# Kernel optimization log

Measured on AMD Instinct MI355X. Metric: run time of the kernel, lower is better.

The kernel has to match this reference:

```python
import jax, jax.numpy as jnp
import numpy as np

NUM_AA, EMB, H = 20, 16, 128
IN1 = 1 + 2 + 4 * EMB  # 67: theta, sin/cos phi, 4-residue context
IN2 = 2 + 2 + 4 * EMB  # 68: sin/cos phi_i, sin/cos phi_{i+1}, context


def setup_inputs() -> dict:
    key = jax.random.key(0)
    ks = jax.random.split(key, 12)
    B, L = 64, 4096
    R = jax.random.normal(ks[0], (B, L, 3), dtype=jnp.float32)
    seq = jax.random.randint(ks[1], (B, L), 0, NUM_AA)
    def lin(k, i, o):
        kw, kb = jax.random.split(k)
        s = 1.0 / np.sqrt(i)
        return (jax.random.uniform(kw, (i, o), jnp.float32, -s, s),
                jax.random.uniform(kb, (o,), jnp.float32, -s, s))
    emb = jax.random.normal(ks[2], (NUM_AA, EMB), dtype=jnp.float32)
    tp_W1, tp_b1 = lin(ks[3], IN1, H)
    tp_W2, tp_b2 = lin(ks[4], H, H)
    tp_W3, tp_b3 = lin(ks[5], H, 1)
    pp_W1, pp_b1 = lin(ks[6], IN2, H)
    pp_W2, pp_b2 = lin(ks[7], H, H)
    pp_W3, pp_b3 = lin(ks[8], H, 1)
    return dict(R=R, seq=seq, emb=emb,
                tp_W1=tp_W1, tp_b1=tp_b1, tp_W2=tp_W2, tp_b2=tp_b2, tp_W3=tp_W3, tp_b3=tp_b3,
                pp_W1=pp_W1, pp_b1=pp_b1, pp_W2=pp_W2, pp_b2=pp_b2, pp_W3=pp_W3, pp_b3=pp_b3)


def _mlp(x, W1, b1, W2, b2, W3, b3):
    h = jax.nn.relu(x @ W1 + b1)
    h = jax.nn.relu(h @ W2 + b2)
    return x @ 0.0 if False else h @ W3 + b3


def _bond_angles(R):
    # angle at residue i+1 of triplet (i, i+1, i+2) -> (B, L-2)
    u1 = R[:, :-2] - R[:, 1:-1]
    u2 = R[:, 2:] - R[:, 1:-1]
    c = jnp.cross(u1, u2)
    return jnp.arctan2(jnp.linalg.norm(c, axis=-1), jnp.sum(u1 * u2, axis=-1))


def _torsions(R):
    # dihedral of quadruplet (i..i+3) -> (B, L-3)
    b1 = R[:, 1:-2] - R[:, :-3]
    b2 = R[:, 2:-1] - R[:, 1:-2]
    b3 = R[:, 3:] - R[:, 2:-1]
    n1 = jnp.cross(b1, b2)
    n2 = jnp.cross(b2, b3)
    b2n = b2 / (jnp.linalg.norm(b2, axis=-1, keepdims=True) + 1e-8)
    x = jnp.sum(n1 * n2, axis=-1)
    y = jnp.sum(jnp.cross(n1, n2) * b2n, axis=-1)
    return jnp.arctan2(y, x)


def reference(R, seq, emb,
              tp_W1, tp_b1, tp_W2, tp_b2, tp_W3, tp_b3,
              pp_W1, pp_b1, pp_W2, pp_b2, pp_W3, pp_b3):
    B, L, _ = R.shape
    e = emb[seq]                                   # (B, L, EMB)
    theta = _bond_angles(R)                        # (B, L-2)
    phi = _torsions(R)                             # (B, L-3)
    sc_phi = jnp.stack([jnp.sin(phi), jnp.cos(phi)], axis=-1)  # (B, L-3, 2)
    theta_in = jnp.cos(theta[:, :L - 3])           # use_cos_theta=True
    ctx = jnp.concatenate([e[:, :-3], e[:, 1:-2], e[:, 2:-1], e[:, 3:]], axis=-1)  # (B, L-3, 4*EMB)
    x1 = jnp.concatenate([theta_in[..., None], sc_phi, ctx], axis=-1)  # (B, L-3, 67)
    E1 = _mlp(x1, tp_W1, tp_b1, tp_W2, tp_b2, tp_W3, tp_b3)[..., 0].sum(axis=1)
    x2 = jnp.concatenate([sc_phi[:, :-1], sc_phi[:, 1:], ctx[:, :-1]], axis=-1)    # (B, L-4, 68)
    E2 = _mlp(x2, pp_W1, pp_b1, pp_W2, pp_b2, pp_W3, pp_b3)[..., 0].sum(axis=1)
    return E1 + E2
```

## Files before the change

### kernel.cpp

```cpp
#include <hip/hip_runtime.h>

#define L_   4096
#define LIM0 4093
#define LIM1 4092

typedef short s16x8 __attribute__((ext_vector_type(8)));
typedef float f32x4 __attribute__((ext_vector_type(4)));

__device__ __forceinline__ unsigned short f2bf(float f) {
    union { float f; unsigned int u; } v; v.f = f;
    unsigned int r = v.u + 0x7FFFu + ((v.u >> 16) & 1u);
    return (unsigned short)(r >> 16);
}

__device__ __forceinline__ unsigned int cvt_pk_bf16(float lo, float hi) {
    unsigned int r;
    asm("v_cvt_pk_bf16_f32 %0, %1, %2" : "=v"(r) : "v"(lo), "v"(hi));
    return r;
}

struct F3 { float x, y, z; };
__device__ __forceinline__ F3 ld3(const float* p) { return F3{p[0], p[1], p[2]}; }
__device__ __forceinline__ F3 sub3(F3 a, F3 b) { return F3{a.x-b.x, a.y-b.y, a.z-b.z}; }
__device__ __forceinline__ F3 cross3(F3 a, F3 b) {
    return F3{a.y*b.z - a.z*b.y, a.z*b.x - a.x*b.z, a.x*b.y - a.y*b.x};
}
__device__ __forceinline__ float dot3(F3 a, F3 b) { return a.x*b.x + a.y*b.y + a.z*b.z; }

__device__ __forceinline__ void torsion(F3 a, F3 b, F3 c, F3 d, float& sn, float& cs) {
    F3 v1 = sub3(b, a), v2 = sub3(c, b), v3 = sub3(d, c);
    F3 n1 = cross3(v1, v2), n2 = cross3(v2, v3);
    float x = dot3(n1, n2);
    F3 m = cross3(n1, n2);
    float bn = sqrtf(dot3(v2, v2)) + 1e-8f;
    float y = dot3(m, v2) / bn;
    float inv = rsqrtf(x*x + y*y + 1e-30f);
    sn = y * inv; cs = x * inv;
}

#define MFMA16 __builtin_amdgcn_mfma_f32_16x16x32_bf16

__global__ __launch_bounds__(256) void ss_mlp(
    const float* __restrict__ R, const int* __restrict__ seq, const float* __restrict__ emb,
    const float* __restrict__ tpW1, const float* __restrict__ tpb1,
    const float* __restrict__ tpW2, const float* __restrict__ tpb2,
    const float* __restrict__ ppW1, const float* __restrict__ ppb1,
    const float* __restrict__ ppW2, const float* __restrict__ ppb2,
    float* __restrict__ wsp) {

    __shared__ __align__(16) unsigned short H1s[64*128];
    __shared__ __align__(16) uint4 embs4[40];
    __shared__ unsigned int feats[520];

    const int b = blockIdx.y, mode = blockIdx.z, bx = blockIdx.x;
    const int lim = mode ? LIM1 : LIM0;
    const float* W1  = mode ? ppW1 : tpW1;
    const float* Bi1 = mode ? ppb1 : tpb1;
    const float* W2  = mode ? ppW2 : tpW2;
    const float* Bi2 = mode ? ppb2 : tpb2;

    const int t = threadIdx.x;
    const int w = t >> 6, l = t & 63, g = l >> 4, ln = l & 15;
    const int lw = ln & 7;
    const size_t bL = (size_t)b * L_;
    const int base = bx * 256;
    const int* seqb = seq + bL;

    int aa_c[8];
    #pragma unroll
    for (int pt = 0; pt < 4; pt++)
        #pragma unroll
        for (int kk = 0; kk < 2; kk++)
            aa_c[pt*2+kk] = seqb[min(base + pt*16 + ln + kk*2 + (g>>1), L_-1)];

    {
        const int pc = min(base + t, lim - 1);
        const float* Rp = R + ((size_t)(bL + pc)) * 3;
        F3 p0 = ld3(Rp), p1 = ld3(Rp+3), p2 = ld3(Rp+6), p3 = ld3(Rp+9);
        float sp, cp; torsion(p0, p1, p2, p3, sp, cp);
        if (mode == 0) {
            F3 u1 = sub3(p0, p1), u2 = sub3(p2, p1);
            F3 cr = cross3(u1, u2);
            float d = dot3(u1, u2);
            float ct = d * rsqrtf(d*d + dot3(cr, cr) + 1e-30f);
            feats[2*t]   = cvt_pk_bf16(ct, sp);
            feats[2*t+1] = cvt_pk_bf16(cp, 1.0f);
        } else {
            feats[t] = cvt_pk_bf16(sp, cp);
            if (t == 0) {
                const int pc2 = min(base + 256, lim - 1);
                const float* R2 = R + ((size_t)(bL + pc2)) * 3;
                F3 q0 = ld3(R2), q1 = ld3(R2+3), q2 = ld3(R2+6), q3 = ld3(R2+9);
                float s2, c2; torsion(q0, q1, q2, q3, s2, c2);
                feats[256] = cvt_pk_bf16(s2, c2);
            }
        }
    }

    if (t < 40) {
        const float* ep = emb + (t >> 1) * 16 + (t & 1) * 8;
        embs4[t] = make_uint4(cvt_pk_bf16(ep[0], ep[1]), cvt_pk_bf16(ep[2], ep[3]),
                              cvt_pk_bf16(ep[4], ep[5]), cvt_pk_bf16(ep[6], ep[7]));
    }

    s16x8 a1f[2][3]; s16x8 a2f[2][4];
    float bb2[2][4];
    #pragma unroll
    for (int mt = 0; mt < 2; mt++) {
        const int hc = w*32 + mt*16 + ln;
        #pragma unroll
        for (int kk = 0; kk < 3; kk++)
            #pragma unroll
            for (int j = 0; j < 8; j++) {
                const int c = kk*32 + g*8 + j;
                int kp;
                if (mode) kp = (c < 64) ? c + 4 : ((c < 68) ? c - 64 : ((c == 68) ? -2 : -1));
                else      kp = (c < 64) ? c + 3 : ((c < 67) ? c - 64 : ((c == 67) ? -2 : -1));
                float wv = (kp == -1) ? 0.f : ((kp == -2) ? Bi1[hc] : W1[kp*128 + hc]);
                a1f[mt][kk][j] = (short)f2bf(wv);
            }
        #pragma unroll
        for (int kk = 0; kk < 4; kk++)
            #pragma unroll
            for (int j = 0; j < 8; j++)
                a2f[mt][kk][j] = (short)f2bf(W2[(kk*32 + g*8 + j)*128 + hc]);
        #pragma unroll
        for (int i = 0; i < 4; i++) bb2[mt][i] = Bi2[w*32 + mt*16 + g*4 + i];
    }

    __syncthreads();

    float s[2][4] = {{0.f,0.f,0.f,0.f},{0.f,0.f,0.f,0.f}};

    #pragma unroll
    for (int it = 0; it < 4; it++) {
        const int pos0 = base + it*64;

        int aa_n[8];
        if (it < 3) {
            #pragma unroll
            for (int pt = 0; pt < 4; pt++)
                #pragma unroll
                for (int kk = 0; kk < 2; kk++)
                    aa_n[pt*2+kk] = seqb[min(pos0 + 64 + pt*16 + ln + kk*2 + (g>>1), L_-1)];
        }

        #pragma unroll
        for (int pt = 0; pt < 4; pt++) {
            const int row = pt*16 + ln;
            const int fidx = it*64 + row;
            s16x8 b0 = *(const s16x8*)&embs4[aa_c[pt*2+0]*2 + (g&1)];
            s16x8 b1 = *(const s16x8*)&embs4[aa_c[pt*2+1]*2 + (g&1)];
            unsigned int f0, f1, f2c;
            if (mode) { f0 = feats[fidx]; f1 = feats[fidx+1]; f2c = 0x00003F80u; }
            else      { f0 = feats[2*fidx]; f1 = feats[2*fidx+1]; f2c = 0u; }
            const bool gz = (g == 0);
            union { unsigned int u[4]; s16x8 v; } fb;
            fb.u[0] = gz ? f0 : 0u; fb.u[1] = gz ? f1 : 0u;
            fb.u[2] = gz ? f2c : 0u; fb.u[3] = 0u;

            f32x4 c0 = {0.f,0.f,0.f,0.f}, c1 = {0.f,0.f,0.f,0.f};
            c0 = MFMA16(a1f[0][0], b0, c0, 0, 0, 0);
            c1 = MFMA16(a1f[1][0], b0, c1, 0, 0, 0);
            c0 = MFMA16(a1f[0][1], b1, c0, 0, 0, 0);
            c1 = MFMA16(a1f[1][1], b1, c1, 0, 0, 0);
            c0 = MFMA16(a1f[0][2], fb.v, c0, 0, 0, 0);
            c1 = MFMA16(a1f[1][2], fb.v, c1, 0, 0, 0);

            unsigned short* hb = H1s + row*128;
            uint2 u;
            u.x = cvt_pk_bf16(fmaxf(c0[0], 0.f), fmaxf(c0[1], 0.f));
            u.y = cvt_pk_bf16(fmaxf(c0[2], 0.f), fmaxf(c0[3], 0.f));
            *(uint2*)(hb + ((((w*4) + (g>>1)) ^ lw) << 3) + (g&1)*4) = u;
            u.x = cvt_pk_bf16(fmaxf(c1[0], 0.f), fmaxf(c1[1], 0.f));
            u.y = cvt_pk_bf16(fmaxf(c1[2], 0.f), fmaxf(c1[3], 0.f));
            *(uint2*)(hb + ((((w*4 + 2) + (g>>1)) ^ lw) << 3) + (g&1)*4) = u;
        }
        __syncthreads();

        #pragma unroll
        for (int pt = 0; pt < 4; pt++) {
            const int row = pt*16 + ln;
            const unsigned short* hbase = H1s + row*128;
            f32x4 d0 = {0.f,0.f,0.f,0.f}, d1 = {0.f,0.f,0.f,0.f};
            #pragma unroll
            for (int kk = 0; kk < 4; kk++) {
                s16x8 bf = *(const s16x8*)(hbase + (((kk*4 + g) ^ lw) << 3));
                d0 = MFMA16(a2f[0][kk], bf, d0, 0, 0, 0);
                d1 = MFMA16(a2f[1][kk], bf, d1, 0, 0, 0);
            }
            if (pos0 + row < lim) {
                #pragma unroll
                for (int i = 0; i < 4; i++) {
                    s[0][i] += fmaxf(d0[i] + bb2[0][i], 0.f);
                    s[1][i] += fmaxf(d1[i] + bb2[1][i], 0.f);
                }
            }
        }
        __syncthreads();

        if (it < 3) {
            #pragma unroll
            for (int j = 0; j < 8; j++) aa_c[j] = aa_n[j];
        }
    }

    #pragma unroll
    for (int mt = 0; mt < 2; mt++)
        #pragma unroll
        for (int i = 0; i < 4; i++) {
            float v = s[mt][i];
            v += __shfl_xor(v, 1, 64); v += __shfl_xor(v, 2, 64);
            v += __shfl_xor(v, 4, 64); v += __shfl_xor(v, 8, 64);
            s[mt][i] = v;
        }
    if (ln == 0) {
        float* dst = wsp + (((size_t)(b*2 + mode)*16 + bx) << 7) + w*32;
        *(f32x4*)(dst +  0 + g*4) = f32x4{s[0][0], s[0][1], s[0][2], s[0][3]};
        *(f32x4*)(dst + 16 + g*4) = f32x4{s[1][0], s[1][1], s[1][2], s[1][3]};
    }
}

__global__ void ss_finish(const float* __restrict__ wsp,
                          const float* __restrict__ tpW3, const float* __restrict__ tpb3,
                          const float* __restrict__ ppW3, const float* __restrict__ ppb3,
                          float* __restrict__ out) {
    const int b = blockIdx.x, t = threadIdx.x;
    const float* p0 = wsp + ((size_t)(b*2 + 0) * 16) * 128;
    const float* p1 = wsp + ((size_t)(b*2 + 1) * 16) * 128;
    float a0 = 0.f, a1 = 0.f;
    #pragma unroll
    for (int bx = 0; bx < 16; bx++) {
        a0 += p0[bx*128 + t];
        a1 += p1[bx*128 + t];
    }
    float v = a0 * tpW3[t] + a1 * ppW3[t];
    #pragma unroll
    for (int off = 1; off < 64; off <<= 1) v += __shfl_xor(v, off, 64);
    __shared__ float ps[2];
    if ((t & 63) == 0) ps[t >> 6] = v;
    __syncthreads();
    if (t == 0) out[b] = ps[0] + ps[1] + 4093.f * tpb3[0] + 4092.f * ppb3[0];
}

extern "C" void kernel_launch(void* const* d_in, const int* in_sizes, int n_in,
                              void* d_out, int out_size, void* d_ws, size_t ws_size,
                              hipStream_t stream) {
    (void)in_sizes; (void)n_in; (void)out_size; (void)ws_size;
    const float* R    = (const float*)d_in[0];
    const int*   seq  = (const int*)d_in[1];
    const float* emb  = (const float*)d_in[2];
    const float* tpW1 = (const float*)d_in[3];
    const float* tpb1 = (const float*)d_in[4];
    const float* tpW2 = (const float*)d_in[5];
    const float* tpb2 = (const float*)d_in[6];
    const float* tpW3 = (const float*)d_in[7];
    const float* tpb3 = (const float*)d_in[8];
    const float* ppW1 = (const float*)d_in[9];
    const float* ppb1 = (const float*)d_in[10];
    const float* ppW2 = (const float*)d_in[11];
    const float* ppb2 = (const float*)d_in[12];
    const float* ppW3 = (const float*)d_in[13];
    const float* ppb3 = (const float*)d_in[14];
    float* wsp = (float*)d_ws;

    ss_mlp<<<dim3(16, 64, 2), 256, 0, stream>>>(R, seq, emb,
                                                tpW1, tpb1, tpW2, tpb2,
                                                ppW1, ppb1, ppW2, ppb2, wsp);
    ss_finish<<<64, 128, 0, stream>>>(wsp, tpW3, tpb3, ppW3, ppb3, (float*)d_out);
}
```

Measured before the change: 52.34 us.

## Precompute geometry features and bf16 weight fragments in a separate prologue kernel

Adds a pre-pass kernel that computes bond-angle and torsion features once per position into global memory, and converts the embedding table and W1/W2 into per-lane bf16 MFMA fragments. The MLP kernel then loads ready-made fragments and features instead of recomputing torsions and converting weights in every block. It also doubles each block's span to 512 positions, halving the grid and the number of partial sums. The cost is an extra kernel launch, global round-trips for features and fragments, per-row global feature and embedding loads in place of shared-memory reads, and a larger shared H1 buffer.

```diff
diff --git a/kernel.cpp b/kernel.cpp
--- a/kernel.cpp
+++ b/kernel.cpp
@@ -6,12 +6,6 @@
 
 typedef short s16x8 __attribute__((ext_vector_type(8)));
 typedef float f32x4 __attribute__((ext_vector_type(4)));
-
-__device__ __forceinline__ unsigned short f2bf(float f) {
-    union { float f; unsigned int u; } v; v.f = f;
-    unsigned int r = v.u + 0x7FFFu + ((v.u >> 16) & 1u);
-    return (unsigned short)(r >> 16);
-}
 
 __device__ __forceinline__ unsigned int cvt_pk_bf16(float lo, float hi) {
     unsigned int r;
@@ -40,154 +34,158 @@
 
 #define MFMA16 __builtin_amdgcn_mfma_f32_16x16x32_bf16
 
+__global__ __launch_bounds__(256) void ss_pre(
+    const float* __restrict__ R, uint2* __restrict__ featG,
+    const float* __restrict__ emb, uint4* __restrict__ embbfG,
+    const float* __restrict__ tpW1, const float* __restrict__ tpb1,
+    const float* __restrict__ tpW2,
+    const float* __restrict__ ppW1, const float* __restrict__ ppb1,
+    const float* __restrict__ ppW2,
+    uint4* __restrict__ wfragG) {
+    const int t = threadIdx.x;
+    if (blockIdx.x == 16) {
+        if (blockIdx.y != 0) return;
+        if (t < 40) {
+            const float* ep = emb + (t >> 1) * 16 + (t & 1) * 8;
+            embbfG[t] = make_uint4(cvt_pk_bf16(ep[0], ep[1]), cvt_pk_bf16(ep[2], ep[3]),
+                                   cvt_pk_bf16(ep[4], ep[5]), cvt_pk_bf16(ep[6], ep[7]));
+        }
+        for (int F = t; F < 7168; F += 256) {
+            int l = F & 63, q = F >> 6;
+            int kkL = q % 7; q /= 7;
+            int mt = q & 1; q >>= 1;
+            int w = q & 3, mode = q >> 2;
+            int g = l >> 4, ln = l & 15;
+            int hc = w*32 + mt*16 + ln;
+            const float* W1  = mode ? ppW1 : tpW1;
+            const float* Bi1 = mode ? ppb1 : tpb1;
+            const float* W2  = mode ? ppW2 : tpW2;
+            float v[8];
+            #pragma unroll
+            for (int j = 0; j < 8; j++) {
+                if (kkL < 3) {
+                    int c = kkL*32 + g*8 + j;
+                    int kp;
+                    if (mode) kp = (c < 64) ? c + 4 : ((c < 68) ? c - 64 : ((c == 68) ? -2 : -1));
+                    else      kp = (c < 64) ? c + 3 : ((c == 64) ? 0 : ((c == 65) ? -2 :
+                                   ((c == 66) ? 1 : ((c == 67) ? 2 : -1))));
+                    v[j] = (kp == -1) ? 0.f : ((kp == -2) ? Bi1[hc] : W1[kp*128 + hc]);
+                } else {
+                    v[j] = W2[((kkL - 3)*32 + g*8 + j)*128 + hc];
+                }
+            }
+            wfragG[F] = make_uint4(cvt_pk_bf16(v[0], v[1]), cvt_pk_bf16(v[2], v[3]),
+                                   cvt_pk_bf16(v[4], v[5]), cvt_pk_bf16(v[6], v[7]));
+        }
+        return;
+    }
+    const int p = blockIdx.x * 256 + t;
+    const int b = blockIdx.y;
+    if (p >= LIM0) return;
+    const float* Rp = R + ((size_t)(b * L_ + p)) * 3;
+    F3 p0 = ld3(Rp), p1 = ld3(Rp + 3), p2 = ld3(Rp + 6), p3 = ld3(Rp + 9);
+    F3 u1 = sub3(p0, p1), u2 = sub3(p2, p1);
+    F3 cr = cross3(u1, u2);
+    float d = dot3(u1, u2);
+    float ct = d * rsqrtf(d * d + dot3(cr, cr) + 1e-30f);
+    float sp, cp; torsion(p0, p1, p2, p3, sp, cp);
+    featG[(size_t)b * L_ + p] = make_uint2(cvt_pk_bf16(ct, 1.0f), cvt_pk_bf16(sp, cp));
+}
+
 __global__ __launch_bounds__(256) void ss_mlp(
-    const float* __restrict__ R, const int* __restrict__ seq, const float* __restrict__ emb,
-    const float* __restrict__ tpW1, const float* __restrict__ tpb1,
-    const float* __restrict__ tpW2, const float* __restrict__ tpb2,
-    const float* __restrict__ ppW1, const float* __restrict__ ppb1,
-    const float* __restrict__ ppW2, const float* __restrict__ ppb2,
+    const int* __restrict__ seq, const uint2* __restrict__ featG,
+    const uint4* __restrict__ embbfG, const uint4* __restrict__ wfragG,
+    const float* __restrict__ tpb2, const float* __restrict__ ppb2,
     float* __restrict__ wsp) {
 
-    __shared__ __align__(16) unsigned short H1s[64*128];
-    __shared__ __align__(16) uint4 embs4[40];
-    __shared__ unsigned int feats[520];
+    __shared__ __align__(16) unsigned short H1s[128*128];
 
     const int b = blockIdx.y, mode = blockIdx.z, bx = blockIdx.x;
     const int lim = mode ? LIM1 : LIM0;
-    const float* W1  = mode ? ppW1 : tpW1;
-    const float* Bi1 = mode ? ppb1 : tpb1;
-    const float* W2  = mode ? ppW2 : tpW2;
     const float* Bi2 = mode ? ppb2 : tpb2;
 
     const int t = threadIdx.x;
     const int w = t >> 6, l = t & 63, g = l >> 4, ln = l & 15;
-    const int lw = ln & 7;
+    const int lw = ln & 7, g2 = g >> 1, gh = g & 1;
     const size_t bL = (size_t)b * L_;
-    const int base = bx * 256;
-    const int* seqb = seq + bL;
-
-    int aa_c[8];
-    #pragma unroll
-    for (int pt = 0; pt < 4; pt++)
-        #pragma unroll
-        for (int kk = 0; kk < 2; kk++)
-            aa_c[pt*2+kk] = seqb[min(base + pt*16 + ln + kk*2 + (g>>1), L_-1)];
-
+    const int base = bx * 512;
+
+    s16x8 fr[2][7];
     {
-        const int pc = min(base + t, lim - 1);
-        const float* Rp = R + ((size_t)(bL + pc)) * 3;
-        F3 p0 = ld3(Rp), p1 = ld3(Rp+3), p2 = ld3(Rp+6), p3 = ld3(Rp+9);
-        float sp, cp; torsion(p0, p1, p2, p3, sp, cp);
-        if (mode == 0) {
-            F3 u1 = sub3(p0, p1), u2 = sub3(p2, p1);
-            F3 cr = cross3(u1, u2);
-            float d = dot3(u1, u2);
-            float ct = d * rsqrtf(d*d + dot3(cr, cr) + 1e-30f);
-            feats[2*t]   = cvt_pk_bf16(ct, sp);
-            feats[2*t+1] = cvt_pk_bf16(cp, 1.0f);
-        } else {
-            feats[t] = cvt_pk_bf16(sp, cp);
-            if (t == 0) {
-                const int pc2 = min(base + 256, lim - 1);
-                const float* R2 = R + ((size_t)(bL + pc2)) * 3;
-                F3 q0 = ld3(R2), q1 = ld3(R2+3), q2 = ld3(R2+6), q3 = ld3(R2+9);
-                float s2, c2; torsion(q0, q1, q2, q3, s2, c2);
-                feats[256] = cvt_pk_bf16(s2, c2);
-            }
-        }
-    }
-
-    if (t < 40) {
-        const float* ep = emb + (t >> 1) * 16 + (t & 1) * 8;
-        embs4[t] = make_uint4(cvt_pk_bf16(ep[0], ep[1]), cvt_pk_bf16(ep[2], ep[3]),
-                              cvt_pk_bf16(ep[4], ep[5]), cvt_pk_bf16(ep[6], ep[7]));
-    }
-
-    s16x8 a1f[2][3]; s16x8 a2f[2][4];
+        const uint4* wf = wfragG + (size_t)(mode*4 + w) * (2*7*64);
+        #pragma unroll
+        for (int mt = 0; mt < 2; mt++)
+            #pragma unroll
+            for (int kkL = 0; kkL < 7; kkL++)
+                fr[mt][kkL] = *(const s16x8*)(wf + (mt*7 + kkL)*64 + l);
+    }
     float bb2[2][4];
     #pragma unroll
-    for (int mt = 0; mt < 2; mt++) {
-        const int hc = w*32 + mt*16 + ln;
-        #pragma unroll
-        for (int kk = 0; kk < 3; kk++)
-            #pragma unroll
-            for (int j = 0; j < 8; j++) {
-                const int c = kk*32 + g*8 + j;
-                int kp;
-                if (mode) kp = (c < 64) ? c + 4 : ((c < 68) ? c - 64 : ((c == 68) ? -2 : -1));
-                else      kp = (c < 64) ? c + 3 : ((c < 67) ? c - 64 : ((c == 67) ? -2 : -1));
-                float wv = (kp == -1) ? 0.f : ((kp == -2) ? Bi1[hc] : W1[kp*128 + hc]);
-                a1f[mt][kk][j] = (short)f2bf(wv);
-            }
-        #pragma unroll
-        for (int kk = 0; kk < 4; kk++)
-            #pragma unroll
-            for (int j = 0; j < 8; j++)
-                a2f[mt][kk][j] = (short)f2bf(W2[(kk*32 + g*8 + j)*128 + hc]);
-        #pragma unroll
-        for (int i = 0; i < 4; i++) bb2[mt][i] = Bi2[w*32 + mt*16 + g*4 + i];
-    }
-
-    __syncthreads();
+    for (int mt = 0; mt < 2; mt++)
+        #pragma unroll
+        for (int i = 0; i < 4; i++)
+            bb2[mt][i] = Bi2[w*32 + mt*16 + g*4 + i];
 
     float s[2][4] = {{0.f,0.f,0.f,0.f},{0.f,0.f,0.f,0.f}};
 
-    #pragma unroll
     for (int it = 0; it < 4; it++) {
-        const int pos0 = base + it*64;
-
-        int aa_n[8];
-        if (it < 3) {
-            #pragma unroll
-            for (int pt = 0; pt < 4; pt++)
-                #pragma unroll
-                for (int kk = 0; kk < 2; kk++)
-                    aa_n[pt*2+kk] = seqb[min(pos0 + 64 + pt*16 + ln + kk*2 + (g>>1), L_-1)];
-        }
-
-        #pragma unroll
-        for (int pt = 0; pt < 4; pt++) {
+        const int pos0 = base + it*128;
+
+        int aa[8][2];
+        #pragma unroll
+        for (int pt = 0; pt < 8; pt++)
+            #pragma unroll
+            for (int e = 0; e < 2; e++)
+                aa[pt][e] = seq[bL + min(pos0 + pt*16 + ln + e*2 + g2, L_ - 1)];
+
+        #pragma unroll
+        for (int pt = 0; pt < 8; pt++) {
             const int row = pt*16 + ln;
-            const int fidx = it*64 + row;
-            s16x8 b0 = *(const s16x8*)&embs4[aa_c[pt*2+0]*2 + (g&1)];
-            s16x8 b1 = *(const s16x8*)&embs4[aa_c[pt*2+1]*2 + (g&1)];
-            unsigned int f0, f1, f2c;
-            if (mode) { f0 = feats[fidx]; f1 = feats[fidx+1]; f2c = 0x00003F80u; }
-            else      { f0 = feats[2*fidx]; f1 = feats[2*fidx+1]; f2c = 0u; }
-            const bool gz = (g == 0);
+            const int pos = pos0 + row;
+            s16x8 b0 = *(const s16x8*)(embbfG + aa[pt][0]*2 + gh);
+            s16x8 b1 = *(const s16x8*)(embbfG + aa[pt][1]*2 + gh);
+            uint2 f0 = make_uint2(0u, 0u), f1 = make_uint2(0u, 0u);
+            if (g == 0) {
+                const int pc = min(pos, lim - 1);
+                f0 = featG[bL + pc];
+                if (mode) f1 = featG[bL + pc + 1];
+            }
             union { unsigned int u[4]; s16x8 v; } fb;
-            fb.u[0] = gz ? f0 : 0u; fb.u[1] = gz ? f1 : 0u;
-            fb.u[2] = gz ? f2c : 0u; fb.u[3] = 0u;
-
+            if (mode) {
+                fb.u[0] = f0.y; fb.u[1] = f1.y;
+                fb.u[2] = (g == 0) ? 0x00003F80u : 0u; fb.u[3] = 0u;
+            } else {
+                fb.u[0] = f0.x; fb.u[1] = f0.y; fb.u[2] = 0u; fb.u[3] = 0u;
+            }
             f32x4 c0 = {0.f,0.f,0.f,0.f}, c1 = {0.f,0.f,0.f,0.f};
-            c0 = MFMA16(a1f[0][0], b0, c0, 0, 0, 0);
-            c1 = MFMA16(a1f[1][0], b0, c1, 0, 0, 0);
-            c0 = MFMA16(a1f[0][1], b1, c0, 0, 0, 0);
-            c1 = MFMA16(a1f[1][1], b1, c1, 0, 0, 0);
-            c0 = MFMA16(a1f[0][2], fb.v, c0, 0, 0, 0);
-            c1 = MFMA16(a1f[1][2], fb.v, c1, 0, 0, 0);
+            c0 = MFMA16(fr[0][0], b0,   c0, 0, 0, 0);
+            c1 = MFMA16(fr[1][0], b0,   c1, 0, 0, 0);
+            c0 = MFMA16(fr[0][1], b1,   c0, 0, 0, 0);
+            c1 = MFMA16(fr[1][1], b1,   c1, 0, 0, 0);
+            c0 = MFMA16(fr[0][2], fb.v, c0, 0, 0, 0);
+            c1 = MFMA16(fr[1][2], fb.v, c1, 0, 0, 0);
 
             unsigned short* hb = H1s + row*128;
             uint2 u;
             u.x = cvt_pk_bf16(fmaxf(c0[0], 0.f), fmaxf(c0[1], 0.f));
             u.y = cvt_pk_bf16(fmaxf(c0[2], 0.f), fmaxf(c0[3], 0.f));
-            *(uint2*)(hb + ((((w*4) + (g>>1)) ^ lw) << 3) + (g&1)*4) = u;
+            *(uint2*)(hb + (((w*4 + g2) ^ lw) << 3) + gh*4) = u;
             u.x = cvt_pk_bf16(fmaxf(c1[0], 0.f), fmaxf(c1[1], 0.f));
             u.y = cvt_pk_bf16(fmaxf(c1[2], 0.f), fmaxf(c1[3], 0.f));
-            *(uint2*)(hb + ((((w*4 + 2) + (g>>1)) ^ lw) << 3) + (g&1)*4) = u;
+            *(uint2*)(hb + (((w*4 + 2 + g2) ^ lw) << 3) + gh*4) = u;
         }
         __syncthreads();
 
         #pragma unroll
-        for (int pt = 0; pt < 4; pt++) {
+        for (int pt = 0; pt < 8; pt++) {
             const int row = pt*16 + ln;
             const unsigned short* hbase = H1s + row*128;
             f32x4 d0 = {0.f,0.f,0.f,0.f}, d1 = {0.f,0.f,0.f,0.f};
             #pragma unroll
             for (int kk = 0; kk < 4; kk++) {
                 s16x8 bf = *(const s16x8*)(hbase + (((kk*4 + g) ^ lw) << 3));
-                d0 = MFMA16(a2f[0][kk], bf, d0, 0, 0, 0);
-                d1 = MFMA16(a2f[1][kk], bf, d1, 0, 0, 0);
+                d0 = MFMA16(fr[0][3+kk], bf, d0, 0, 0, 0);
+                d1 = MFMA16(fr[1][3+kk], bf, d1, 0, 0, 0);
             }
             if (pos0 + row < lim) {
                 #pragma unroll
@@ -198,11 +196,6 @@
             }
         }
         __syncthreads();
-
-        if (it < 3) {
-            #pragma unroll
-            for (int j = 0; j < 8; j++) aa_c[j] = aa_n[j];
-        }
     }
 
     #pragma unroll
@@ -215,7 +208,7 @@
             s[mt][i] = v;
         }
     if (ln == 0) {
-        float* dst = wsp + (((size_t)(b*2 + mode)*16 + bx) << 7) + w*32;
+        float* dst = wsp + (((size_t)(b*2 + mode)*8 + bx) << 7) + w*32;
         *(f32x4*)(dst +  0 + g*4) = f32x4{s[0][0], s[0][1], s[0][2], s[0][3]};
         *(f32x4*)(dst + 16 + g*4) = f32x4{s[1][0], s[1][1], s[1][2], s[1][3]};
     }
@@ -226,13 +219,13 @@
                           const float* __restrict__ ppW3, const float* __restrict__ ppb3,
                           float* __restrict__ out) {
     const int b = blockIdx.x, t = threadIdx.x;
-    const float* p0 = wsp + ((size_t)(b*2 + 0) * 16) * 128;
-    const float* p1 = wsp + ((size_t)(b*2 + 1) * 16) * 128;
+    const float* p0 = wsp + (size_t)(b*2 + 0) * 8 * 128;
+    const float* p1 = wsp + (size_t)(b*2 + 1) * 8 * 128;
     float a0 = 0.f, a1 = 0.f;
     #pragma unroll
-    for (int bx = 0; bx < 16; bx++) {
-        a0 += p0[bx*128 + t];
-        a1 += p1[bx*128 + t];
+    for (int k = 0; k < 8; k++) {
+        a0 += p0[k*128 + t];
+        a1 += p1[k*128 + t];
     }
     float v = a0 * tpW3[t] + a1 * ppW3[t];
     #pragma unroll
@@ -262,10 +255,16 @@
     const float* ppb2 = (const float*)d_in[12];
     const float* ppW3 = (const float*)d_in[13];
     const float* ppb3 = (const float*)d_in[14];
-    float* wsp = (float*)d_ws;
-
-    ss_mlp<<<dim3(16, 64, 2), 256, 0, stream>>>(R, seq, emb,
-                                                tpW1, tpb1, tpW2, tpb2,
-                                                ppW1, ppb1, ppW2, ppb2, wsp);
+
+    char* wsb = (char*)d_ws;
+    float* wsp   = (float*)wsb;
+    uint2* featG = (uint2*)(wsb + (512<<10));
+    uint4* embbfG = (uint4*)(wsb + (512<<10) + (2<<20));
+    uint4* wfragG = (uint4*)(wsb + (512<<10) + (2<<20) + 1024);
+
+    ss_pre<<<dim3(17, 64), 256, 0, stream>>>(R, featG, emb, embbfG,
+                                             tpW1, tpb1, tpW2, ppW1, ppb1, ppW2, wfragG);
+    ss_mlp<<<dim3(8, 64, 2), 256, 0, stream>>>(seq, featG, embbfG, wfragG,
+                                               tpb2, ppb2, wsp);
     ss_finish<<<64, 128, 0, stream>>>(wsp, tpW3, tpb3, ppW3, ppb3, (float*)d_out);
 }
```

Measured after the change: 75.60 us. 44.4% more time.
